# Kernel tuning notes

Hardware: AMD Instinct MI355X
Metric: run time of the kernel (lower is better)

Reference implementation:

```python
import jax, jax.numpy as jnp
import numpy as np

D_KEY = 128
INF = 1e9  # stands in for the module's global INF constant


def setup_inputs() -> dict:
    key = jax.random.key(0)
    kq, kk, kv = jax.random.split(key, 3)
    B, S, D = 8, 4096, D_KEY
    return {
        "query": jax.random.normal(kq, (B, S, D), dtype=jnp.float32),
        "keys": jax.random.normal(kk, (B, S, D), dtype=jnp.float32),
        "values": jax.random.normal(kv, (B, S, D), dtype=jnp.float32),
    }


def reference(query, keys, values):
    # dot_products: [B, Sq, Sk]
    scores = jnp.einsum("bqd,bkd->bqk", query, keys)
    S = scores.shape[-1]
    # causal: subtract INF on strict upper triangle (triu(1)), applied BEFORE scaling
    causal = jnp.triu(jnp.ones((S, S), dtype=scores.dtype), 1) * INF
    logits = (scores - causal[None, :, :]) / jnp.asarray(np.sqrt(D_KEY), scores.dtype)
    # legacy F.softmax on 3D transposed tensor == softmax over key axis
    probs = jax.nn.softmax(logits, axis=-1)
    # dropout with p=0.0 is identity
    return jnp.einsum("bqk,bkd->bqd", probs, values)
```

## Files before the change

### kernel.cpp

```cpp
#include <hip/hip_runtime.h>
#include <hip/hip_bf16.h>

#define B_SZ   8
#define S_LEN  4096
#define D_K    128
#define KB     64
#define CH     16
#define NCHUNK 1280

#define KT_STR 136
#define VT_STR 72
#define PT_STR 72

typedef short  short8  __attribute__((ext_vector_type(8)));
typedef float  floatx4 __attribute__((ext_vector_type(4)));

#define EXP2F(x) exp2f(x)

__device__ __forceinline__ unsigned bfround(float x) {
  unsigned u = __builtin_bit_cast(unsigned, x);
  return (u + 0x7fffu + ((u >> 16) & 1u)) >> 16;
}
__device__ __forceinline__ unsigned bfpack2(float a, float b) {
  return bfround(a) | (bfround(b) << 16);
}


__global__ __launch_bounds__(256)
void conv_k(const float* __restrict__ K, unsigned short* __restrict__ Kb) {
  const size_t idx = ((size_t)blockIdx.x * 256 + threadIdx.x) * 8;
  float4 f0 = *(const float4*)(K + idx);
  float4 f1 = *(const float4*)(K + idx + 4);
  uint4 u;
  u.x = bfpack2(f0.x, f0.y);
  u.y = bfpack2(f0.z, f0.w);
  u.z = bfpack2(f1.x, f1.y);
  u.w = bfpack2(f1.z, f1.w);
  *(uint4*)(Kb + idx) = u;
}

__global__ __launch_bounds__(256)
void transp_v(const float* __restrict__ V, unsigned short* __restrict__ Vt) {
  __shared__ float tile[64][65];
  const int t   = threadIdx.x;
  const int bid = blockIdx.x;
  const int b   = bid >> 7;
  const int rem = bid & 127;
  const int kt  = (rem >> 1) * 64;
  const int dt  = (rem & 1) * 64;
  {
    const int c  = (t & 15) * 4;
    const int r0 = t >> 4;
#pragma unroll
    for (int rr = 0; rr < 4; ++rr) {
      const int r = r0 + rr * 16;
      float4 f = *(const float4*)(V + (size_t)(b * S_LEN + kt + r) * D_K + dt + c);
      tile[r][c]     = f.x;
      tile[r][c + 1] = f.y;
      tile[r][c + 2] = f.z;
      tile[r][c + 3] = f.w;
    }
  }
  __syncthreads();
  {
    const int d  = t >> 2;
    const int k0 = (t & 3) * 16;
#pragma unroll
    for (int j = 0; j < 16; j += 8) {
      uint4 u;
      u.x = bfpack2(tile[k0 + j + 0][d], tile[k0 + j + 1][d]);
      u.y = bfpack2(tile[k0 + j + 2][d], tile[k0 + j + 3][d]);
      u.z = bfpack2(tile[k0 + j + 4][d], tile[k0 + j + 5][d]);
      u.w = bfpack2(tile[k0 + j + 6][d], tile[k0 + j + 7][d]);
      *(uint4*)(Vt + (size_t)(b * D_K + dt + d) * S_LEN + kt + k0 + j) = u;
    }
  }
}

__global__ void zero_cnt(int* cnt) { *cnt = 0; }


__global__ __launch_bounds__(128, 2)
void attn_worker(const float* __restrict__ Q, const unsigned short* __restrict__ Kb,
                 const unsigned short* __restrict__ Vt, int* __restrict__ cnt,
                 float* __restrict__ ml, float* __restrict__ pO) {
  __shared__ __align__(16) short Klds[KB * KT_STR];
  __shared__ __align__(16) short Vtlds[D_K * VT_STR];
  __shared__ __align__(16) short Plds[2 * 16 * PT_STR];
  __shared__ int s_chunk;

  const int tid  = threadIdx.x;
  const int lane = tid & 63;
  const int w    = tid >> 6;
  const int l15  = lane & 15;
  const int quad = lane >> 4;

  const int kr0 = tid >> 4;
  const int kc  = (tid & 15) * 8;
  const int vr0 = tid >> 3;
  const int vc  = (tid & 7) * 8;

  const float CSC = 0.12752041f;

  for (;;) {
    if (tid == 0) s_chunk = atomicAdd(cnt, 1);
    __syncthreads();
    const int c = s_chunk;
    if (c >= NCHUNK) break;

    int b, qi, j;
    if (c < 800) {
      const int r = c >> 3;  b = c & 7;
      if      (r <  4) { qi = 63;               j = r;            }
      else if (r < 52) { qi = 62 - (r-4)/3;     j = (r-4)%3;      }
      else if (r < 84) { qi = 46 - (r-52)/2;    j = (r-52)%2;     }
      else             { qi = 30 - (r-84);      j = 0;            }
    } else {
      const int rc = c - 800;
      const int s  = 15 - (rc >> 5);
      const int t  = rc & 31;
      b  = t & 7;
      qi = s - 1 + 16 * (t >> 3);
      j  = (qi + 1) >> 4;
    }

    const int q0 = qi * 64;
    const int s0 = j * CH;
    const int s1 = min(s0 + CH, qi + 1);

    short8 bq[2][4];
    int qg[2];
#pragma unroll
    for (int sub = 0; sub < 2; ++sub) {
      qg[sub] = q0 + w * 32 + sub * 16 + l15;
      const float* qrow = Q + (size_t)(b * S_LEN + qg[sub]) * D_K + quad * 8;
#pragma unroll
      for (int kd = 0; kd < 4; ++kd) {
        float4 f0 = *(const float4*)(qrow + kd * 32);
        float4 f1 = *(const float4*)(qrow + kd * 32 + 4);
        union { short8 s; unsigned u[4]; } t;
        t.u[0] = bfpack2(f0.x, f0.y);
        t.u[1] = bfpack2(f0.z, f0.w);
        t.u[2] = bfpack2(f1.x, f1.y);
        t.u[3] = bfpack2(f1.z, f1.w);
        bq[sub][kd] = t.s;
      }
    }

    floatx4 acc[2][8];
#pragma unroll
    for (int sub = 0; sub < 2; ++sub)
#pragma unroll
      for (int nc = 0; nc < 8; ++nc) acc[sub][nc] = (floatx4){0.f, 0.f, 0.f, 0.f};
    float m_run[2] = {-1e30f, -1e30f}, l_run[2] = {0.f, 0.f};

    const unsigned short* kbase = Kb + (size_t)(b * S_LEN) * D_K;
    const unsigned short* vbase = Vt + (size_t)(b * D_K) * S_LEN;

    for (int s = s0; s < s1; ++s) {
      const int kt = s * KB;

#pragma unroll
      for (int i = 0; i < 8; ++i) {
        uint4 u = *(const uint4*)(kbase + (size_t)(kt + kr0 + i * 8) * D_K + kc);
        *(uint4*)(&Klds[(kr0 + i * 8) * KT_STR + kc]) = u;
      }
#pragma unroll
      for (int i = 0; i < 8; ++i) {
        uint4 u = *(const uint4*)(vbase + (size_t)(vr0 + i * 16) * S_LEN + kt + vc);
        *(uint4*)(&Vtlds[(vr0 + i * 16) * VT_STR + vc]) = u;
      }
      __syncthreads();

      floatx4 st[2][4];
#pragma unroll
      for (int kf = 0; kf < 4; ++kf) {
        floatx4 c0 = (floatx4){0.f, 0.f, 0.f, 0.f};
        floatx4 c1 = (floatx4){0.f, 0.f, 0.f, 0.f};
#pragma unroll
        for (int kd = 0; kd < 4; ++kd) {
          short8 a = *(const short8*)(&Klds[(kf * 16 + l15) * KT_STR + kd * 32 + quad * 8]);
          c0 = __builtin_amdgcn_mfma_f32_16x16x32_bf16(a, bq[0][kd], c0, 0, 0, 0);
          c1 = __builtin_amdgcn_mfma_f32_16x16x32_bf16(a, bq[1][kd], c1, 0, 0, 0);
        }
        st[0][kf] = c0;
        st[1][kf] = c1;
      }

      if (s == qi) {
#pragma unroll
        for (int sub = 0; sub < 2; ++sub)
#pragma unroll
          for (int kf = 0; kf < 4; ++kf)
#pragma unroll
            for (int r = 0; r < 4; ++r) {
              int key = kt + kf * 16 + quad * 4 + r;
              if (key > qg[sub]) st[sub][kf][r] = -1e30f;
            }
      }

      short8 pa[2][2];
#pragma unroll
      for (int sub = 0; sub < 2; ++sub) {
        float mx = st[sub][0][0];
#pragma unroll
        for (int kf = 0; kf < 4; ++kf)
#pragma unroll
          for (int r = 0; r < 4; ++r) mx = fmaxf(mx, st[sub][kf][r]);
        mx = fmaxf(mx, __shfl_xor(mx, 16, 64));
        mx = fmaxf(mx, __shfl_xor(mx, 32, 64));
        const float m_new = fmaxf(m_run[sub], mx);
        const float alpha = EXP2F((m_run[sub] - m_new) * CSC);

        float p[4][4];
        float tsum = 0.f;
#pragma unroll
        for (int kf = 0; kf < 4; ++kf)
#pragma unroll
          for (int r = 0; r < 4; ++r) {
            p[kf][r] = EXP2F((st[sub][kf][r] - m_new) * CSC);
            tsum += p[kf][r];
          }
        tsum += __shfl_xor(tsum, 16, 64);
        tsum += __shfl_xor(tsum, 32, 64);
        l_run[sub] = l_run[sub] * alpha + tsum;
        m_run[sub] = m_new;

#pragma unroll
        for (int r = 0; r < 4; ++r) {
          const float ar = __shfl(alpha, quad * 4 + r, 64);
#pragma unroll
          for (int nc = 0; nc < 8; ++nc) acc[sub][nc][r] *= ar;
        }

        short* pw = &Plds[(w * 16 + l15) * PT_STR];
#pragma unroll
        for (int kf = 0; kf < 4; ++kf) {
          uint2 u;
          u.x = bfpack2(p[kf][0], p[kf][1]);
          u.y = bfpack2(p[kf][2], p[kf][3]);
          *(uint2*)(&pw[kf * 16 + quad * 4]) = u;
        }
        __asm__ __volatile__("" ::: "memory");
        pa[sub][0] = *(const short8*)(&pw[quad * 8]);
        pa[sub][1] = *(const short8*)(&pw[32 + quad * 8]);
        __asm__ __volatile__("" ::: "memory");
      }

#pragma unroll
      for (int nc = 0; nc < 8; ++nc) {
        short8 bv0 = *(const short8*)(&Vtlds[(nc * 16 + l15) * VT_STR + quad * 8]);
        short8 bv1 = *(const short8*)(&Vtlds[(nc * 16 + l15) * VT_STR + 32 + quad * 8]);
        acc[0][nc] = __builtin_amdgcn_mfma_f32_16x16x32_bf16(pa[0][0], bv0, acc[0][nc], 0, 0, 0);
        acc[0][nc] = __builtin_amdgcn_mfma_f32_16x16x32_bf16(pa[0][1], bv1, acc[0][nc], 0, 0, 0);
        acc[1][nc] = __builtin_amdgcn_mfma_f32_16x16x32_bf16(pa[1][0], bv0, acc[1][nc], 0, 0, 0);
        acc[1][nc] = __builtin_amdgcn_mfma_f32_16x16x32_bf16(pa[1][1], bv1, acc[1][nc], 0, 0, 0);
      }
      __syncthreads();
    }

    const int slot = ((b << 6) | qi) * 4 + j;
    float* po = pO + (size_t)slot * 8192;
#pragma unroll
    for (int sub = 0; sub < 2; ++sub) {
#pragma unroll
      for (int r = 0; r < 4; ++r) {
        const int qrow = w * 32 + sub * 16 + quad * 4 + r;
        float* op = po + qrow * D_K + l15;
#pragma unroll
        for (int nc = 0; nc < 8; ++nc) op[nc * 16] = acc[sub][nc][r];
      }
      if (quad == 0) {
        const int qrow = w * 32 + sub * 16 + l15;
        ml[(size_t)slot * 128 + qrow * 2]     = m_run[sub];
        ml[(size_t)slot * 128 + qrow * 2 + 1] = l_run[sub];
      }
    }
  }
}


__global__ __launch_bounds__(256)
void attn_combine(const float* __restrict__ ml, const float* __restrict__ pO,
                  float* __restrict__ O) {
  const int t   = blockIdx.x;
  const int b   = t >> 6;
  const int qi  = t & 63;
  const int ncb = ((qi + 1) + 15) >> 4;
  const float CSC = 0.12752041f;

  const int tid = threadIdx.x;
  const int q   = tid >> 2;
  const int dp  = (tid & 3) * 32;

  float m[4], l[4];
  float M = -1e30f;
  for (int jj = 0; jj < ncb; ++jj) {
    const int slot = t * 4 + jj;
    m[jj] = ml[(size_t)slot * 128 + q * 2];
    l[jj] = ml[(size_t)slot * 128 + q * 2 + 1];
    M = fmaxf(M, m[jj]);
  }
  float wgt[4], L = 0.f;
  for (int jj = 0; jj < ncb; ++jj) {
    wgt[jj] = EXP2F((m[jj] - M) * CSC);
    L += wgt[jj] * l[jj];
  }
  const float inv = 1.0f / L;

  float4 out[8];
#pragma unroll
  for (int v = 0; v < 8; ++v) out[v] = make_float4(0.f, 0.f, 0.f, 0.f);
  for (int jj = 0; jj < ncb; ++jj) {
    const float* src = pO + (size_t)(t * 4 + jj) * 8192 + q * D_K + dp;
    const float wj = wgt[jj];
#pragma unroll
    for (int v = 0; v < 8; ++v) {
      float4 f = *(const float4*)(src + v * 4);
      out[v].x += wj * f.x;  out[v].y += wj * f.y;
      out[v].z += wj * f.z;  out[v].w += wj * f.w;
    }
  }
  float* dst = O + (size_t)(b * S_LEN + qi * 64 + q) * D_K + dp;
#pragma unroll
  for (int v = 0; v < 8; ++v) {
    float4 f = make_float4(out[v].x * inv, out[v].y * inv, out[v].z * inv, out[v].w * inv);
    *(float4*)(dst + v * 4) = f;
  }
}


__global__ __launch_bounds__(256, 2)
void attn_fwd_fb(const float* __restrict__ Q, const float* __restrict__ K,
                 const float* __restrict__ V, float* __restrict__ O) {
  __shared__ __align__(16) short Klds[KB * KT_STR];
  __shared__ __align__(16) short Vtlds[D_K * VT_STR];
  __shared__ __align__(16) short Plds[4 * 16 * PT_STR];

  const int tid  = threadIdx.x;
  const int lane = tid & 63;
  const int w    = tid >> 6;
  const int l15  = lane & 15;
  const int quad = lane >> 4;

  const int bid = blockIdx.x;
  const int b   = bid & 7;
  const int qi  = 63 - (bid >> 3);
  const int q0  = qi * 64;

  const float CSC = 0.12752041f;

  const int    qg   = q0 + w * 16 + l15;
  const float* qrow = Q + (size_t)(b * S_LEN + qg) * D_K + quad * 8;
  short8 bq[4];
#pragma unroll
  for (int kd = 0; kd < 4; ++kd) {
    float4 f0 = *(const float4*)(qrow + kd * 32);
    float4 f1 = *(const float4*)(qrow + kd * 32 + 4);
    union { short8 s; unsigned u[4]; } t;
    t.u[0] = bfpack2(f0.x, f0.y);
    t.u[1] = bfpack2(f0.z, f0.w);
    t.u[2] = bfpack2(f1.x, f1.y);
    t.u[3] = bfpack2(f1.z, f1.w);
    bq[kd] = t.s;
  }

  floatx4 acc[8];
#pragma unroll
  for (int nc = 0; nc < 8; ++nc) acc[nc] = (floatx4){0.f, 0.f, 0.f, 0.f};
  float m_run = -1e30f, l_run = 0.f;

  const int d4 = tid & 31;
  const int kq = tid >> 5;
  const int nsteps = qi + 1;

  for (int s = 0; s < nsteps; ++s) {
    const int kt = s * KB;
#pragma unroll
    for (int r2 = 0; r2 < 2; ++r2) {
      const int row = r2 * 32 + kq * 4;
      const float* kp = K + (size_t)(b * S_LEN + kt + row) * D_K + d4 * 4;
      const float* vp = V + (size_t)(b * S_LEN + kt + row) * D_K + d4 * 4;
      float4 fk[4], fv[4];
#pragma unroll
      for (int i = 0; i < 4; ++i) {
        fk[i] = *(const float4*)(kp + i * D_K);
        fv[i] = *(const float4*)(vp + i * D_K);
      }
#pragma unroll
      for (int i = 0; i < 4; ++i) {
        uint2 u;
        u.x = bfpack2(fk[i].x, fk[i].y);
        u.y = bfpack2(fk[i].z, fk[i].w);
        *(uint2*)(&Klds[(row + i) * KT_STR + d4 * 4]) = u;
      }
#pragma unroll
      for (int c = 0; c < 4; ++c) {
        float e0 = ((const float*)&fv[0])[c];
        float e1 = ((const float*)&fv[1])[c];
        float e2 = ((const float*)&fv[2])[c];
        float e3 = ((const float*)&fv[3])[c];
        uint2 u;
        u.x = bfpack2(e0, e1);
        u.y = bfpack2(e2, e3);
        *(uint2*)(&Vtlds[(d4 * 4 + c) * VT_STR + row]) = u;
      }
    }
    __syncthreads();

    floatx4 st[4];
#pragma unroll
    for (int kf = 0; kf < 4; ++kf) {
      floatx4 c = (floatx4){0.f, 0.f, 0.f, 0.f};
#pragma unroll
      for (int kd = 0; kd < 4; ++kd) {
        short8 a = *(const short8*)(&Klds[(kf * 16 + l15) * KT_STR + kd * 32 + quad * 8]);
        c = __builtin_amdgcn_mfma_f32_16x16x32_bf16(a, bq[kd], c, 0, 0, 0);
      }
      st[kf] = c;
    }

    if (s == nsteps - 1) {
#pragma unroll
      for (int kf = 0; kf < 4; ++kf)
#pragma unroll
        for (int r = 0; r < 4; ++r) {
          int key = kt + kf * 16 + quad * 4 + r;
          if (key > qg) st[kf][r] = -1e30f;
        }
    }

    float mx = st[0][0];
#pragma unroll
    for (int kf = 0; kf < 4; ++kf)
#pragma unroll
      for (int r = 0; r < 4; ++r) mx = fmaxf(mx, st[kf][r]);
    mx = fmaxf(mx, __shfl_xor(mx, 16, 64));
    mx = fmaxf(mx, __shfl_xor(mx, 32, 64));
    const float m_new = fmaxf(m_run, mx);
    const float alpha = EXP2F((m_run - m_new) * CSC);

    float p[4][4];
    float tsum = 0.f;
#pragma unroll
    for (int kf = 0; kf < 4; ++kf)
#pragma unroll
      for (int r = 0; r < 4; ++r) {
        p[kf][r] = EXP2F((st[kf][r] - m_new) * CSC);
        tsum += p[kf][r];
      }
    tsum += __shfl_xor(tsum, 16, 64);
    tsum += __shfl_xor(tsum, 32, 64);
    l_run = l_run * alpha + tsum;
    m_run = m_new;

#pragma unroll
    for (int r = 0; r < 4; ++r) {
      const float ar = __shfl(alpha, quad * 4 + r, 64);
#pragma unroll
      for (int nc = 0; nc < 8; ++nc) acc[nc][r] *= ar;
    }

    short* pw = &Plds[(w * 16 + l15) * PT_STR];
#pragma unroll
    for (int kf = 0; kf < 4; ++kf) {
      uint2 u;
      u.x = bfpack2(p[kf][0], p[kf][1]);
      u.y = bfpack2(p[kf][2], p[kf][3]);
      *(uint2*)(&pw[kf * 16 + quad * 4]) = u;
    }
    __asm__ __volatile__("" ::: "memory");
    short8 pa0 = *(const short8*)(&pw[quad * 8]);
    short8 pa1 = *(const short8*)(&pw[32 + quad * 8]);

#pragma unroll
    for (int nc = 0; nc < 8; ++nc) {
      short8 bv0 = *(const short8*)(&Vtlds[(nc * 16 + l15) * VT_STR + quad * 8]);
      acc[nc] = __builtin_amdgcn_mfma_f32_16x16x32_bf16(pa0, bv0, acc[nc], 0, 0, 0);
      short8 bv1 = *(const short8*)(&Vtlds[(nc * 16 + l15) * VT_STR + 32 + quad * 8]);
      acc[nc] = __builtin_amdgcn_mfma_f32_16x16x32_bf16(pa1, bv1, acc[nc], 0, 0, 0);
    }
    __syncthreads();
  }

#pragma unroll
  for (int r = 0; r < 4; ++r) {
    const float lr  = __shfl(l_run, quad * 4 + r, 64);
    const float inv = 1.0f / lr;
    const int qout  = q0 + w * 16 + quad * 4 + r;
    float* op = O + (size_t)(b * S_LEN + qout) * D_K + l15;
#pragma unroll
    for (int nc = 0; nc < 8; ++nc) op[nc * 16] = acc[nc][r] * inv;
  }
}


extern "C" void kernel_launch(void* const* d_in, const int* in_sizes, int n_in,
                              void* d_out, int out_size, void* d_ws, size_t ws_size,
                              hipStream_t stream) {
  const float* Q = (const float*)d_in[0];
  const float* K = (const float*)d_in[1];
  const float* V = (const float*)d_in[2];
  float* O = (float*)d_out;

  const size_t elems = (size_t)B_SZ * S_LEN * D_K;

  const size_t off_ml = 256;
  const size_t off_po = off_ml + 2048ull * 128 * 4;
  const size_t off_kb = off_po + 2048ull * 8192 * 4;
  const size_t off_vt = off_kb + elems * 2;
  const size_t need   = off_vt + elems * 2;

  if (ws_size >= need) {
    char* ws = (char*)d_ws;
    int*            cnt = (int*)ws;
    float*          ml  = (float*)(ws + off_ml);
    float*          po  = (float*)(ws + off_po);
    unsigned short* Kb  = (unsigned short*)(ws + off_kb);
    unsigned short* Vt  = (unsigned short*)(ws + off_vt);

    zero_cnt<<<dim3(1), dim3(1), 0, stream>>>(cnt);
    conv_k<<<dim3((unsigned)(elems / 8 / 256)), dim3(256), 0, stream>>>(K, Kb);
    transp_v<<<dim3(B_SZ * (S_LEN / 64) * (D_K / 64)), dim3(256), 0, stream>>>(V, Vt);
    attn_worker<<<dim3(1024), dim3(128), 0, stream>>>(Q, Kb, Vt, cnt, ml, po);
    attn_combine<<<dim3(512), dim3(256), 0, stream>>>(ml, po, O);
  } else {
    attn_fwd_fb<<<dim3(512), dim3(256), 0, stream>>>(Q, K, V, O);
  }
}
```

Measured before the change: 194.4 us.

## Fuse prepass kernels, register-prefetch K/V tiles, and combine splits in last-arriving worker

Merges K conversion, V transpose and counter zeroing into one prepass launch. In the attention worker, the next K/V tile is held in registers so its global loads overlap the current tile's compute. The separate combine kernel is removed: a per-tile atomic counter lets the last split to finish merge the partial outputs and write O directly. This cuts launch count and tail gaps, in exchange for more register pressure and threadfence/atomic synchronisation inside the worker.

```diff
diff --git a/kernel.cpp b/kernel.cpp
--- a/kernel.cpp
+++ b/kernel.cpp
@@ -27,67 +27,73 @@
 
 
 __global__ __launch_bounds__(256)
-void conv_k(const float* __restrict__ K, unsigned short* __restrict__ Kb) {
-  const size_t idx = ((size_t)blockIdx.x * 256 + threadIdx.x) * 8;
-  float4 f0 = *(const float4*)(K + idx);
-  float4 f1 = *(const float4*)(K + idx + 4);
-  uint4 u;
-  u.x = bfpack2(f0.x, f0.y);
-  u.y = bfpack2(f0.z, f0.w);
-  u.z = bfpack2(f1.x, f1.y);
-  u.w = bfpack2(f1.z, f1.w);
-  *(uint4*)(Kb + idx) = u;
-}
-
-__global__ __launch_bounds__(256)
-void transp_v(const float* __restrict__ V, unsigned short* __restrict__ Vt) {
+void prepass(const float* __restrict__ K, const float* __restrict__ V,
+             unsigned short* __restrict__ Kb, unsigned short* __restrict__ Vt,
+             int* __restrict__ cnt) {
   __shared__ float tile[64][65];
+  const int bid = blockIdx.x;
   const int t   = threadIdx.x;
-  const int bid = blockIdx.x;
-  const int b   = bid >> 7;
-  const int rem = bid & 127;
-  const int kt  = (rem >> 1) * 64;
-  const int dt  = (rem & 1) * 64;
-  {
-    const int c  = (t & 15) * 4;
-    const int r0 = t >> 4;
-#pragma unroll
-    for (int rr = 0; rr < 4; ++rr) {
-      const int r = r0 + rr * 16;
-      float4 f = *(const float4*)(V + (size_t)(b * S_LEN + kt + r) * D_K + dt + c);
-      tile[r][c]     = f.x;
-      tile[r][c + 1] = f.y;
-      tile[r][c + 2] = f.z;
-      tile[r][c + 3] = f.w;
-    }
-  }
-  __syncthreads();
-  {
-    const int d  = t >> 2;
-    const int k0 = (t & 3) * 16;
-#pragma unroll
-    for (int j = 0; j < 16; j += 8) {
-      uint4 u;
-      u.x = bfpack2(tile[k0 + j + 0][d], tile[k0 + j + 1][d]);
-      u.y = bfpack2(tile[k0 + j + 2][d], tile[k0 + j + 3][d]);
-      u.z = bfpack2(tile[k0 + j + 4][d], tile[k0 + j + 5][d]);
-      u.w = bfpack2(tile[k0 + j + 6][d], tile[k0 + j + 7][d]);
-      *(uint4*)(Vt + (size_t)(b * D_K + dt + d) * S_LEN + kt + k0 + j) = u;
-    }
+
+  if (bid < 2048) {
+    const size_t idx = ((size_t)bid * 256 + t) * 8;
+    float4 f0 = *(const float4*)(K + idx);
+    float4 f1 = *(const float4*)(K + idx + 4);
+    uint4 u;
+    u.x = bfpack2(f0.x, f0.y);
+    u.y = bfpack2(f0.z, f0.w);
+    u.z = bfpack2(f1.x, f1.y);
+    u.w = bfpack2(f1.z, f1.w);
+    *(uint4*)(Kb + idx) = u;
+  } else if (bid < 3072) {
+    const int vb  = bid - 2048;
+    const int b   = vb >> 7;
+    const int rem = vb & 127;
+    const int kt  = (rem >> 1) * 64;
+    const int dt  = (rem & 1) * 64;
+    {
+      const int c  = (t & 15) * 4;
+      const int r0 = t >> 4;
+#pragma unroll
+      for (int rr = 0; rr < 4; ++rr) {
+        const int r = r0 + rr * 16;
+        float4 f = *(const float4*)(V + (size_t)(b * S_LEN + kt + r) * D_K + dt + c);
+        tile[r][c]     = f.x;
+        tile[r][c + 1] = f.y;
+        tile[r][c + 2] = f.z;
+        tile[r][c + 3] = f.w;
+      }
+    }
+    __syncthreads();
+    {
+      const int d  = t >> 2;
+      const int k0 = (t & 3) * 16;
+#pragma unroll
+      for (int j = 0; j < 16; j += 8) {
+        uint4 u;
+        u.x = bfpack2(tile[k0 + j + 0][d], tile[k0 + j + 1][d]);
+        u.y = bfpack2(tile[k0 + j + 2][d], tile[k0 + j + 3][d]);
+        u.z = bfpack2(tile[k0 + j + 4][d], tile[k0 + j + 5][d]);
+        u.w = bfpack2(tile[k0 + j + 6][d], tile[k0 + j + 7][d]);
+        *(uint4*)(Vt + (size_t)(b * D_K + dt + d) * S_LEN + kt + k0 + j) = u;
+      }
+    }
+  } else {
+    for (int i = t; i < 1024; i += 256) cnt[i] = 0;
   }
 }
-
-__global__ void zero_cnt(int* cnt) { *cnt = 0; }
 
 
 __global__ __launch_bounds__(128, 2)
 void attn_worker(const float* __restrict__ Q, const unsigned short* __restrict__ Kb,
                  const unsigned short* __restrict__ Vt, int* __restrict__ cnt,
-                 float* __restrict__ ml, float* __restrict__ pO) {
+                 float* __restrict__ ml, float* __restrict__ pO,
+                 float* __restrict__ O) {
   __shared__ __align__(16) short Klds[KB * KT_STR];
   __shared__ __align__(16) short Vtlds[D_K * VT_STR];
   __shared__ __align__(16) short Plds[2 * 16 * PT_STR];
-  __shared__ int s_chunk;
+  __shared__ int s_comm[2];
+
+  int* tile_done = cnt + 256;
 
   const int tid  = threadIdx.x;
   const int lane = tid & 63;
@@ -103,9 +109,10 @@
   const float CSC = 0.12752041f;
 
   for (;;) {
-    if (tid == 0) s_chunk = atomicAdd(cnt, 1);
-    __syncthreads();
-    const int c = s_chunk;
+    if (tid == 0) s_comm[0] = atomicAdd(&cnt[0], 1);
+    __syncthreads();
+    const int c = s_comm[0];
+    __syncthreads();
     if (c >= NCHUNK) break;
 
     int b, qi, j;
@@ -117,10 +124,10 @@
       else             { qi = 30 - (r-84);      j = 0;            }
     } else {
       const int rc = c - 800;
-      const int s  = 15 - (rc >> 5);
-      const int t  = rc & 31;
-      b  = t & 7;
-      qi = s - 1 + 16 * (t >> 3);
+      const int sd = 15 - (rc >> 5);
+      const int tt = rc & 31;
+      b  = tt & 7;
+      qi = sd - 1 + 16 * (tt >> 3);
       j  = (qi + 1) >> 4;
     }
 
@@ -157,20 +164,37 @@
     const unsigned short* kbase = Kb + (size_t)(b * S_LEN) * D_K;
     const unsigned short* vbase = Vt + (size_t)(b * D_K) * S_LEN;
 
+    uint4 rk[8], rv[8];
+    {
+      const int kt = s0 * KB;
+#pragma unroll
+      for (int i = 0; i < 8; ++i)
+        rk[i] = *(const uint4*)(kbase + (size_t)(kt + kr0 + i * 8) * D_K + kc);
+#pragma unroll
+      for (int i = 0; i < 8; ++i)
+        rv[i] = *(const uint4*)(vbase + (size_t)(vr0 + i * 16) * S_LEN + kt + vc);
+    }
+
     for (int s = s0; s < s1; ++s) {
+#pragma unroll
+      for (int i = 0; i < 8; ++i)
+        *(uint4*)(&Klds[(kr0 + i * 8) * KT_STR + kc]) = rk[i];
+#pragma unroll
+      for (int i = 0; i < 8; ++i)
+        *(uint4*)(&Vtlds[(vr0 + i * 16) * VT_STR + vc]) = rv[i];
+      __syncthreads();
+
+      if (s + 1 < s1) {
+        const int kt2 = (s + 1) * KB;
+#pragma unroll
+        for (int i = 0; i < 8; ++i)
+          rk[i] = *(const uint4*)(kbase + (size_t)(kt2 + kr0 + i * 8) * D_K + kc);
+#pragma unroll
+        for (int i = 0; i < 8; ++i)
+          rv[i] = *(const uint4*)(vbase + (size_t)(vr0 + i * 16) * S_LEN + kt2 + vc);
+      }
+
       const int kt = s * KB;
-
-#pragma unroll
-      for (int i = 0; i < 8; ++i) {
-        uint4 u = *(const uint4*)(kbase + (size_t)(kt + kr0 + i * 8) * D_K + kc);
-        *(uint4*)(&Klds[(kr0 + i * 8) * KT_STR + kc]) = u;
-      }
-#pragma unroll
-      for (int i = 0; i < 8; ++i) {
-        uint4 u = *(const uint4*)(vbase + (size_t)(vr0 + i * 16) * S_LEN + kt + vc);
-        *(uint4*)(&Vtlds[(vr0 + i * 16) * VT_STR + vc]) = u;
-      }
-      __syncthreads();
 
       floatx4 st[2][4];
 #pragma unroll
@@ -259,7 +283,8 @@
       __syncthreads();
     }
 
-    const int slot = ((b << 6) | qi) * 4 + j;
+    const int tile = (b << 6) | qi;
+    const int slot = tile * 4 + j;
     float* po = pO + (size_t)slot * 8192;
 #pragma unroll
     for (int sub = 0; sub < 2; ++sub) {
@@ -276,56 +301,54 @@
         ml[(size_t)slot * 128 + qrow * 2 + 1] = l_run[sub];
       }
     }
-  }
-}
-
-
-__global__ __launch_bounds__(256)
-void attn_combine(const float* __restrict__ ml, const float* __restrict__ pO,
-                  float* __restrict__ O) {
-  const int t   = blockIdx.x;
-  const int b   = t >> 6;
-  const int qi  = t & 63;
-  const int ncb = ((qi + 1) + 15) >> 4;
-  const float CSC = 0.12752041f;
-
-  const int tid = threadIdx.x;
-  const int q   = tid >> 2;
-  const int dp  = (tid & 3) * 32;
-
-  float m[4], l[4];
-  float M = -1e30f;
-  for (int jj = 0; jj < ncb; ++jj) {
-    const int slot = t * 4 + jj;
-    m[jj] = ml[(size_t)slot * 128 + q * 2];
-    l[jj] = ml[(size_t)slot * 128 + q * 2 + 1];
-    M = fmaxf(M, m[jj]);
-  }
-  float wgt[4], L = 0.f;
-  for (int jj = 0; jj < ncb; ++jj) {
-    wgt[jj] = EXP2F((m[jj] - M) * CSC);
-    L += wgt[jj] * l[jj];
-  }
-  const float inv = 1.0f / L;
-
-  float4 out[8];
-#pragma unroll
-  for (int v = 0; v < 8; ++v) out[v] = make_float4(0.f, 0.f, 0.f, 0.f);
-  for (int jj = 0; jj < ncb; ++jj) {
-    const float* src = pO + (size_t)(t * 4 + jj) * 8192 + q * D_K + dp;
-    const float wj = wgt[jj];
-#pragma unroll
-    for (int v = 0; v < 8; ++v) {
-      float4 f = *(const float4*)(src + v * 4);
-      out[v].x += wj * f.x;  out[v].y += wj * f.y;
-      out[v].z += wj * f.z;  out[v].w += wj * f.w;
-    }
-  }
-  float* dst = O + (size_t)(b * S_LEN + qi * 64 + q) * D_K + dp;
-#pragma unroll
-  for (int v = 0; v < 8; ++v) {
-    float4 f = make_float4(out[v].x * inv, out[v].y * inv, out[v].z * inv, out[v].w * inv);
-    *(float4*)(dst + v * 4) = f;
+
+    const int ncb = ((qi + 1) + 15) >> 4;
+    __syncthreads();
+    if (tid == 0) {
+      __threadfence();
+      const int old = atomicAdd(&tile_done[tile], 1);
+      s_comm[1] = (old == ncb - 1) ? 1 : 0;
+    }
+    __syncthreads();
+    if (s_comm[1]) {
+      __threadfence();
+      const int q   = tid >> 1;
+      const int dh  = (tid & 1) * 64;
+      float m[4], l[4];
+      float M = -1e30f;
+      for (int jj = 0; jj < ncb; ++jj) {
+        m[jj] = ml[(size_t)(tile * 4 + jj) * 128 + q * 2];
+        l[jj] = ml[(size_t)(tile * 4 + jj) * 128 + q * 2 + 1];
+        M = fmaxf(M, m[jj]);
+      }
+      float wgt[4], L = 0.f;
+      for (int jj = 0; jj < ncb; ++jj) {
+        wgt[jj] = EXP2F((m[jj] - M) * CSC);
+        L += wgt[jj] * l[jj];
+      }
+      const float inv = 1.0f / L;
+      float* dst = O + (size_t)(b * S_LEN + qi * 64 + q) * D_K + dh;
+#pragma unroll
+      for (int pp = 0; pp < 4; ++pp) {
+        float4 a0 = make_float4(0.f, 0.f, 0.f, 0.f), a1 = a0, a2 = a0, a3 = a0;
+        for (int jj = 0; jj < ncb; ++jj) {
+          const float* src = pO + (size_t)(tile * 4 + jj) * 8192 + q * D_K + dh + pp * 16;
+          const float wj = wgt[jj];
+          float4 f0 = *(const float4*)(src);
+          float4 f1 = *(const float4*)(src + 4);
+          float4 f2 = *(const float4*)(src + 8);
+          float4 f3 = *(const float4*)(src + 12);
+          a0.x += wj * f0.x; a0.y += wj * f0.y; a0.z += wj * f0.z; a0.w += wj * f0.w;
+          a1.x += wj * f1.x; a1.y += wj * f1.y; a1.z += wj * f1.z; a1.w += wj * f1.w;
+          a2.x += wj * f2.x; a2.y += wj * f2.y; a2.z += wj * f2.z; a2.w += wj * f2.w;
+          a3.x += wj * f3.x; a3.y += wj * f3.y; a3.z += wj * f3.z; a3.w += wj * f3.w;
+        }
+        *(float4*)(dst + pp * 16)      = make_float4(a0.x * inv, a0.y * inv, a0.z * inv, a0.w * inv);
+        *(float4*)(dst + pp * 16 + 4)  = make_float4(a1.x * inv, a1.y * inv, a1.z * inv, a1.w * inv);
+        *(float4*)(dst + pp * 16 + 8)  = make_float4(a2.x * inv, a2.y * inv, a2.z * inv, a2.w * inv);
+        *(float4*)(dst + pp * 16 + 12) = make_float4(a3.x * inv, a3.y * inv, a3.z * inv, a3.w * inv);
+      }
+    }
   }
 }
 
@@ -505,7 +528,7 @@
 
   const size_t elems = (size_t)B_SZ * S_LEN * D_K;
 
-  const size_t off_ml = 256;
+  const size_t off_ml = 4096;
   const size_t off_po = off_ml + 2048ull * 128 * 4;
   const size_t off_kb = off_po + 2048ull * 8192 * 4;
   const size_t off_vt = off_kb + elems * 2;
@@ -519,11 +542,8 @@
     unsigned short* Kb  = (unsigned short*)(ws + off_kb);
     unsigned short* Vt  = (unsigned short*)(ws + off_vt);
 
-    zero_cnt<<<dim3(1), dim3(1), 0, stream>>>(cnt);
-    conv_k<<<dim3((unsigned)(elems / 8 / 256)), dim3(256), 0, stream>>>(K, Kb);
-    transp_v<<<dim3(B_SZ * (S_LEN / 64) * (D_K / 64)), dim3(256), 0, stream>>>(V, Vt);
-    attn_worker<<<dim3(1024), dim3(128), 0, stream>>>(Q, Kb, Vt, cnt, ml, po);
-    attn_combine<<<dim3(512), dim3(256), 0, stream>>>(ml, po, O);
+    prepass<<<dim3(3073), dim3(256), 0, stream>>>(K, V, Kb, Vt, cnt);
+    attn_worker<<<dim3(1024), dim3(128), 0, stream>>>(Q, Kb, Vt, cnt, ml, po, O);
   } else {
     attn_fwd_fb<<<dim3(512), dim3(256), 0, stream>>>(Q, K, V, O);
   }
```

New measurement: 454.9 us. 134% more time.
